# Performance work log

Hardware: AMD Instinct MI355X
Metric: run time of the kernel (lower is better)

The kernel has to match this reference:

```python
import jax, jax.numpy as jnp
import numpy as np

B, C, H, W = 8, 256, 64, 64
S = H * W  # dim_spatial = 4096
DQK = 256
DV = 256


def setup_inputs() -> dict:
    key = jax.random.key(0)
    k1, k2, k3, k4, k5 = jax.random.split(key, 5)
    queries = jax.random.normal(k1, (B, DQK, H, W), dtype=jnp.float32)
    keys = jax.random.normal(k2, (B, DQK, H, W), dtype=jnp.float32)
    values = jax.random.normal(k3, (B, DV, H, W), dtype=jnp.float32)
    q_pos = jax.random.normal(k4, (1, S, DQK), dtype=jnp.float32) * 0.05  # 'random_normal' init
    k_pos = jax.random.normal(k5, (1, S, DQK), dtype=jnp.float32) * 0.05
    return {"queries": queries, "keys": keys, "values": values, "q_pos": q_pos, "k_pos": k_pos}


def reference(queries, keys, values, q_pos, k_pos):
    scale = DQK ** (-0.5)
    # NCHW -> (B, S, C)
    q = jnp.transpose(queries, (0, 2, 3, 1)).reshape(-1, S, DQK) + q_pos
    k = jnp.transpose(keys, (0, 2, 3, 1)).reshape(-1, S, DQK) + k_pos
    v = jnp.transpose(values, (0, 2, 3, 1)).reshape(-1, S, DV)
    dots = jnp.einsum('bqd,bkd->bqk', q, k) * scale  # (B, S, S)
    attn = jax.nn.softmax(dots, axis=-1)
    out = jnp.einsum('bqk,bkd->bqd', attn, v)  # (B, S, DV)
    out = jnp.transpose(out, (0, 2, 1)).reshape(values.shape)  # (B, DV, H, W)
    return out
```

## Files before the change

### kernel.cpp

```cpp
#include <hip/hip_runtime.h>
#include <hip/hip_bf16.h>

#define B_N   8
#define S_N   4096
#define D_N   256
#define QBLK  128
#define KVBLK 32
#define NCH   (S_N / KVBLK)
#define IMGSZ 16384
#define SCALE_Q (0.0625f * 1.4426950408889634f)

typedef __attribute__((ext_vector_type(8)))  short bf16x8;
typedef __attribute__((ext_vector_type(16))) float f32x16;

__device__ __forceinline__ void async16(const char* g, char* l) {
  __builtin_amdgcn_global_load_lds(
      (const __attribute__((address_space(1))) void*)g,
      (__attribute__((address_space(3))) void*)l, 16, 0, 0);
}

__device__ __forceinline__ unsigned cvt_pk_bf16(float lo, float hi) {
  unsigned r;
  asm("v_cvt_pk_bf16_f32 %0, %1, %2" : "=v"(r) : "v"(lo), "v"(hi));
  return r;
}
__device__ __forceinline__ void swap32(unsigned& a, unsigned& b) {
  asm("v_permlane32_swap_b32 %0, %1" : "+v"(a), "+v"(b));
}
__device__ __forceinline__ float xhalf_max(float x) {
  float a = x, b = x;
  asm("" : "+v"(b));
  asm("v_permlane32_swap_b32 %0, %1" : "+v"(a), "+v"(b));
  return fmaxf(a, b);
}
__device__ __forceinline__ float xhalf_add(float x) {
  float a = x, b = x;
  asm("" : "+v"(b));
  asm("v_permlane32_swap_b32 %0, %1" : "+v"(a), "+v"(b));
  return a + b;
}
__device__ __forceinline__ float exp2_fast(float x) {
  float r;
  asm("v_exp_f32 %0, %1" : "=v"(r) : "v"(x));
  return r;
}
__device__ __forceinline__ unsigned short bf16_bits(float x) {
  union { __hip_bfloat16 h; unsigned short u; } cvt;
  cvt.h = __float2bfloat16(x);
  return cvt.u;
}

__global__ void prep_qk(const float* __restrict__ src, const float* __restrict__ pos,
                        __hip_bfloat16* __restrict__ dst, float mul) {
  __shared__ float tile[64][65];
  const int b  = blockIdx.z;
  const int s0 = blockIdx.x * 64;
  const int c0 = blockIdx.y * 64;
  const int t  = threadIdx.x;
  const int x  = t & 63;
  const int y4 = t >> 6;
  const float* sp = src + ((size_t)b * D_N + c0) * S_N + s0;
#pragma unroll
  for (int i = 0; i < 16; ++i) {
    int c = y4 + i * 4;
    tile[c][x] = sp[(size_t)c * S_N + x];
  }
  __syncthreads();
  __hip_bfloat16* dp = dst + ((size_t)b * S_N + s0) * D_N + c0;
  const float* pp = pos + (size_t)s0 * D_N + c0;
#pragma unroll
  for (int i = 0; i < 16; ++i) {
    int s = y4 + i * 4;
    float v = (tile[x][s] + pp[(size_t)s * D_N + x]) * mul;
    dp[(size_t)s * D_N + x] = __float2bfloat16(v);
  }
}

__global__ void prep_kimg(const float* __restrict__ src, const float* __restrict__ pos,
                          char* __restrict__ img) {
  __shared__ float tile[64][65];
  const int b  = blockIdx.z;
  const int s0 = blockIdx.x * 64;
  const int c0 = blockIdx.y * 64;
  const int t  = threadIdx.x;
  const int x  = t & 63;
  const int y4 = t >> 6;
  const float* sp = src + ((size_t)b * D_N + c0) * S_N + s0;
#pragma unroll
  for (int i = 0; i < 16; ++i) {
    int c = y4 + i * 4;
    tile[c][x] = sp[(size_t)c * S_N + x];
  }
  __syncthreads();
  const float* pp = pos + (size_t)s0 * D_N + c0;
#pragma unroll
  for (int i = 0; i < 16; ++i) {
    int srow = y4 + i * 4;
    int d    = c0 + x;
    float v  = tile[x][srow] + pp[(size_t)srow * D_N + x];
    int s    = s0 + srow;
    int ch   = s >> 5;
    char* dst = img + ((size_t)(b * NCH + ch)) * IMGSZ
                + (d >> 4) * 1024 + (s & 31) * 32 + (d & 15) * 2;
    *reinterpret_cast<__hip_bfloat16*>(dst) = __float2bfloat16(v);
  }
}

struct alignas(16) bf8s { __hip_bfloat16 v[8]; };
__global__ void prep_vimg(const float* __restrict__ src, char* __restrict__ img) {
  const int ch = blockIdx.x;
  const int b  = blockIdx.y;
  const int t  = threadIdx.x;
  char* ib = img + ((size_t)(b * NCH + ch)) * IMGSZ;
#pragma unroll
  for (int i = 0; i < 4; ++i) {
    int idx = i * 256 + t;
    int kf  = idx >> 9;
    int d   = (idx >> 1) & 255;
    int hf  = idx & 1;
    const float* vs = src + ((size_t)b * D_N + d) * S_N + ch * KVBLK + kf * 16 + hf * 8;
    float4 a = *reinterpret_cast<const float4*>(vs);
    float4 c = *reinterpret_cast<const float4*>(vs + 4);
    bf8s w;
    w.v[0] = __float2bfloat16(a.x); w.v[1] = __float2bfloat16(a.y);
    w.v[2] = __float2bfloat16(a.z); w.v[3] = __float2bfloat16(a.w);
    w.v[4] = __float2bfloat16(c.x); w.v[5] = __float2bfloat16(c.y);
    w.v[6] = __float2bfloat16(c.z); w.v[7] = __float2bfloat16(c.w);
    *reinterpret_cast<bf8s*>(ib + kf * 8192 + d * 32 + hf * 16) = w;
  }
}

#define LDS_BYTES 65536

__global__ __launch_bounds__(256, 2) void attn_kernel(
    const __hip_bfloat16* __restrict__ Qb, const char* __restrict__ Kt,
    const char* __restrict__ Vt, __hip_bfloat16* __restrict__ P0,
    float2* __restrict__ mlbuf, float* __restrict__ out) {
  __shared__ __align__(16) char lds[LDS_BYTES];

  const int tid  = threadIdx.x;
  const int wave = tid >> 6;
  const int lane = tid & 63;
  const int l31  = lane & 31;
  const int h    = lane >> 5;
  const int lofs = l31 * 32 + h * 16;

  const int lin = blockIdx.x;
  const int b   = lin & 7;
  const int kvh = (lin >> 3) & 1;
  const int qt  = lin >> 4;
  const int q0  = qt * QBLK + wave * 32;
  const int t0  = kvh * (NCH / 2);

  bf16x8 qf[16];
  {
    const __hip_bfloat16* qp = Qb + ((size_t)b * S_N + q0 + l31) * D_N + h * 8;
#pragma unroll
    for (int kc = 0; kc < 16; ++kc)
      qf[kc] = *reinterpret_cast<const bf16x8*>(qp + kc * 16);
  }

  f32x16 o[8];
#pragma unroll
  for (int df = 0; df < 8; ++df)
#pragma unroll
    for (int r = 0; r < 16; ++r) o[df][r] = 0.f;
  float m_ = -1e30f, l_ = 0.f;

  const char* kimgB = Kt + (size_t)b * NCH * IMGSZ;
  const char* vimgB = Vt + (size_t)b * NCH * IMGSZ;

  auto COMPUTE = [&](const char* Kbase, const char* Vbase) {
    f32x16 se;
#pragma unroll
    for (int r = 0; r < 16; ++r) se[r] = 0.f;
    {
      const char* kr = Kbase + lofs;
      __builtin_amdgcn_s_setprio(1);
#pragma unroll
      for (int kc = 0; kc < 16; ++kc) {
        bf16x8 kf8 = *reinterpret_cast<const bf16x8*>(kr + kc * 1024);
        se = __builtin_amdgcn_mfma_f32_32x32x16_bf16(kf8, qf[kc], se, 0, 0, 0);
      }
      __builtin_amdgcn_s_setprio(0);
    }

    float t8[8];
#pragma unroll
    for (int i = 0; i < 8; ++i) t8[i] = fmaxf(se[i], se[i + 8]);
    float pm = fmaxf(fmaxf(fmaxf(t8[0], t8[1]), fmaxf(t8[2], t8[3])),
                     fmaxf(fmaxf(t8[4], t8[5]), fmaxf(t8[6], t8[7])));
    float pmax = xhalf_max(pm);

    if (!__all(pmax <= m_ + 11.54f)) {
      float mn = fmaxf(m_, pmax);
      float al = exp2_fast(m_ - mn);
      m_ = mn;
      l_ *= al;
#pragma unroll
      for (int df = 0; df < 8; ++df)
#pragma unroll
        for (int r = 0; r < 16; ++r) o[df][r] *= al;
    }
#pragma unroll
    for (int r = 0; r < 16; ++r) se[r] = exp2_fast(se[r] - m_);
    float s8[8];
#pragma unroll
    for (int i = 0; i < 8; ++i) s8[i] = se[i] + se[i + 8];
    float rs = ((s8[0] + s8[1]) + (s8[2] + s8[3])) + ((s8[4] + s8[5]) + (s8[6] + s8[7]));
    l_ += xhalf_add(rs);

    union U8 { unsigned u[4]; bf16x8 v; };
    U8 pb[2];
    {
      unsigned u0 = cvt_pk_bf16(se[0],  se[1]);
      unsigned v0 = cvt_pk_bf16(se[4],  se[5]);
      swap32(u0, v0);
      unsigned u1 = cvt_pk_bf16(se[2],  se[3]);
      unsigned v1 = cvt_pk_bf16(se[6],  se[7]);
      swap32(u1, v1);
      pb[0].u[0] = u0; pb[0].u[1] = u1; pb[0].u[2] = v0; pb[0].u[3] = v1;
      unsigned u2 = cvt_pk_bf16(se[8],  se[9]);
      unsigned v2 = cvt_pk_bf16(se[12], se[13]);
      swap32(u2, v2);
      unsigned u3 = cvt_pk_bf16(se[10], se[11]);
      unsigned v3 = cvt_pk_bf16(se[14], se[15]);
      swap32(u3, v3);
      pb[1].u[0] = u2; pb[1].u[1] = u3; pb[1].u[2] = v2; pb[1].u[3] = v3;
    }

    {
      const char* vr = Vbase + lofs;
      __builtin_amdgcn_s_setprio(1);
#pragma unroll
      for (int df = 0; df < 8; ++df) {
        bf16x8 vf0 = *reinterpret_cast<const bf16x8*>(vr + df * 1024);
        bf16x8 vf1 = *reinterpret_cast<const bf16x8*>(vr + 8192 + df * 1024);
        o[df] = __builtin_amdgcn_mfma_f32_32x32x16_bf16(vf0, pb[0].v, o[df], 0, 0, 0);
        o[df] = __builtin_amdgcn_mfma_f32_32x32x16_bf16(vf1, pb[1].v, o[df], 0, 0, 0);
      }
      __builtin_amdgcn_s_setprio(0);
    }
  };

  for (int t = 0; t < NCH / 4; ++t) {
    __syncthreads();
    {
      const int ch = t0 + 2 * t + (wave & 1);
      const char* s = (wave < 2 ? kimgB : vimgB) + (size_t)ch * IMGSZ;
      char* dstb = lds + (wave < 2 ? 0 : 32768) + (wave & 1) * 16384;
#pragma unroll
      for (int c = 0; c < 16; ++c)
        async16(s + c * 1024 + lane * 16, dstb + c * 1024);
    }
    __syncthreads();

    COMPUTE(lds,         lds + 32768);
    COMPUTE(lds + 16384, lds + 49152);
  }

  if (h == 0)
    mlbuf[(size_t)(kvh * B_N + b) * S_N + q0 + l31] = make_float2(m_, l_);
  if (kvh) {
    float* pdst = out + (size_t)b * D_N * S_N + q0 + l31;
#pragma unroll
    for (int df = 0; df < 8; ++df)
#pragma unroll
      for (int r = 0; r < 16; ++r) {
        int d = df * 32 + (r & 3) + 8 * (r >> 2) + 4 * h;
        __builtin_nontemporal_store(o[df][r], pdst + (size_t)d * S_N);
      }
  } else {
    unsigned short* pdst = reinterpret_cast<unsigned short*>(P0)
                           + (size_t)b * D_N * S_N + q0 + l31;
#pragma unroll
    for (int df = 0; df < 8; ++df)
#pragma unroll
      for (int r = 0; r < 16; ++r) {
        int d = df * 32 + (r & 3) + 8 * (r >> 2) + 4 * h;
        __builtin_nontemporal_store(bf16_bits(o[df][r]), pdst + (size_t)d * S_N);
      }
  }
}

__global__ void merge_w(const float2* __restrict__ mlbuf, float2* __restrict__ wbuf) {
  int i = blockIdx.x * 256 + threadIdx.x;
  float2 a = mlbuf[i];
  float2 c = mlbuf[(size_t)B_N * S_N + i];
  float ms = fmaxf(a.x, c.x);
  float c0 = exp2f(a.x - ms), c1 = exp2f(c.x - ms);
  float inv = 1.0f / (c0 * a.y + c1 * c.y);
  wbuf[i] = make_float2(c0 * inv, c1 * inv);
}

__global__ void merge_o(const __hip_bfloat16* __restrict__ P0,
                        const float2* __restrict__ wbuf, float* __restrict__ out) {
  int i = blockIdx.x * 256 + threadIdx.x;
  ushort4 p0u = reinterpret_cast<const ushort4*>(P0)[i];
  float4 p1 = reinterpret_cast<float4*>(out)[i];
  int b  = i >> 18;
  int s4 = i & (S_N / 4 - 1);
  const float2* wb = wbuf + (size_t)b * S_N + s4 * 4;
  float2 w0 = wb[0], w1 = wb[1], w2 = wb[2], w3 = wb[3];
  union { unsigned short u; __hip_bfloat16 h; } cvt;
  float4 r;
  cvt.u = p0u.x; r.x = w0.x * __bfloat162float(cvt.h) + w0.y * p1.x;
  cvt.u = p0u.y; r.y = w1.x * __bfloat162float(cvt.h) + w1.y * p1.y;
  cvt.u = p0u.z; r.z = w2.x * __bfloat162float(cvt.h) + w2.y * p1.z;
  cvt.u = p0u.w; r.w = w3.x * __bfloat162float(cvt.h) + w3.y * p1.w;
  reinterpret_cast<float4*>(out)[i] = r;
}

extern "C" void kernel_launch(void* const* d_in, const int* in_sizes, int n_in,
                              void* d_out, int out_size, void* d_ws, size_t ws_size,
                              hipStream_t stream) {
  const float* queries = (const float*)d_in[0];
  const float* keys    = (const float*)d_in[1];
  const float* values  = (const float*)d_in[2];
  const float* q_pos   = (const float*)d_in[3];
  const float* k_pos   = (const float*)d_in[4];
  float* out = (float*)d_out;

  const size_t per = (size_t)B_N * S_N * D_N;
  __hip_bfloat16* Qb = (__hip_bfloat16*)d_ws;
  char*   Kt    = (char*)d_ws + per * 2;
  char*   Vt    = Kt + per * 2;
  __hip_bfloat16* P0 = (__hip_bfloat16*)(Vt + per * 2);
  float2* mlbuf = (float2*)((char*)P0 + per * 2);
  float2* wbuf  = mlbuf + (size_t)2 * B_N * S_N;

  prep_qk  <<<dim3(S_N / 64, D_N / 64, B_N), 256, 0, stream>>>(queries, q_pos, Qb, SCALE_Q);
  prep_kimg<<<dim3(S_N / 64, D_N / 64, B_N), 256, 0, stream>>>(keys,    k_pos, Kt);
  prep_vimg<<<dim3(NCH, B_N), 256, 0, stream>>>(values, Vt);
  attn_kernel<<<dim3((S_N / QBLK) * B_N * 2), 256, 0, stream>>>(Qb, Kt, Vt, P0, mlbuf, out);
  merge_w<<<dim3(B_N * S_N / 256), 256, 0, stream>>>(mlbuf, wbuf);
  merge_o<<<dim3((unsigned)(per / 4 / 256)), 256, 0, stream>>>(P0, wbuf, out);
}
```

Baseline: 192.5 us.

## Read V fragments directly from global memory and fuse merge weight computation

The attention kernel now stages only the K tiles in LDS and loads V operand fragments straight from global memory (through L2) inside the PV matmul, which halves LDS use from 64KB to 32KB. Freeing LDS could allow more blocks per CU, at the cost of exposing global-load latency directly in front of the PV MFMAs. The priority boost around the PV loop is also removed. The separate merge_w kernel is folded into merge_o, which now recomputes the rescale weights per element from the saved max/sum pairs, removing one launch and the intermediate weight buffer.

```diff
diff --git a/kernel.cpp b/kernel.cpp
--- a/kernel.cpp
+++ b/kernel.cpp
@@ -130,7 +130,7 @@
   }
 }
 
-#define LDS_BYTES 65536
+#define LDS_BYTES 32768
 
 __global__ __launch_bounds__(256, 2) void attn_kernel(
     const __hip_bfloat16* __restrict__ Qb, const char* __restrict__ Kt,
@@ -170,7 +170,7 @@
   const char* kimgB = Kt + (size_t)b * NCH * IMGSZ;
   const char* vimgB = Vt + (size_t)b * NCH * IMGSZ;
 
-  auto COMPUTE = [&](const char* Kbase, const char* Vbase) {
+  auto COMPUTE = [&](const char* Kbase, const char* vg) {
     f32x16 se;
 #pragma unroll
     for (int r = 0; r < 16; ++r) se[r] = 0.f;
@@ -230,8 +230,7 @@
     }
 
     {
-      const char* vr = Vbase + lofs;
-      __builtin_amdgcn_s_setprio(1);
+      const char* vr = vg + lofs;
 #pragma unroll
       for (int df = 0; df < 8; ++df) {
         bf16x8 vf0 = *reinterpret_cast<const bf16x8*>(vr + df * 1024);
@@ -239,24 +238,23 @@
         o[df] = __builtin_amdgcn_mfma_f32_32x32x16_bf16(vf0, pb[0].v, o[df], 0, 0, 0);
         o[df] = __builtin_amdgcn_mfma_f32_32x32x16_bf16(vf1, pb[1].v, o[df], 0, 0, 0);
       }
-      __builtin_amdgcn_s_setprio(0);
     }
   };
 
   for (int t = 0; t < NCH / 4; ++t) {
     __syncthreads();
     {
-      const int ch = t0 + 2 * t + (wave & 1);
-      const char* s = (wave < 2 ? kimgB : vimgB) + (size_t)ch * IMGSZ;
-      char* dstb = lds + (wave < 2 ? 0 : 32768) + (wave & 1) * 16384;
-#pragma unroll
-      for (int c = 0; c < 16; ++c)
-        async16(s + c * 1024 + lane * 16, dstb + c * 1024);
+      const char* s = kimgB + (size_t)(t0 + 2 * t) * IMGSZ;
+#pragma unroll
+      for (int c = 0; c < 8; ++c) {
+        int seg = wave * 8 + c;
+        async16(s + seg * 1024 + lane * 16, lds + seg * 1024);
+      }
     }
     __syncthreads();
 
-    COMPUTE(lds,         lds + 32768);
-    COMPUTE(lds + 16384, lds + 49152);
+    COMPUTE(lds,         vimgB + (size_t)(t0 + 2 * t)     * IMGSZ);
+    COMPUTE(lds + 16384, vimgB + (size_t)(t0 + 2 * t + 1) * IMGSZ);
   }
 
   if (h == 0)
@@ -283,32 +281,31 @@
   }
 }
 
-__global__ void merge_w(const float2* __restrict__ mlbuf, float2* __restrict__ wbuf) {
-  int i = blockIdx.x * 256 + threadIdx.x;
-  float2 a = mlbuf[i];
-  float2 c = mlbuf[(size_t)B_N * S_N + i];
-  float ms = fmaxf(a.x, c.x);
-  float c0 = exp2f(a.x - ms), c1 = exp2f(c.x - ms);
-  float inv = 1.0f / (c0 * a.y + c1 * c.y);
-  wbuf[i] = make_float2(c0 * inv, c1 * inv);
-}
-
 __global__ void merge_o(const __hip_bfloat16* __restrict__ P0,
-                        const float2* __restrict__ wbuf, float* __restrict__ out) {
+                        const float2* __restrict__ mlbuf, float* __restrict__ out) {
   int i = blockIdx.x * 256 + threadIdx.x;
   ushort4 p0u = reinterpret_cast<const ushort4*>(P0)[i];
   float4 p1 = reinterpret_cast<float4*>(out)[i];
   int b  = i >> 18;
   int s4 = i & (S_N / 4 - 1);
-  const float2* wb = wbuf + (size_t)b * S_N + s4 * 4;
-  float2 w0 = wb[0], w1 = wb[1], w2 = wb[2], w3 = wb[3];
+  const float2* ml0 = mlbuf + (size_t)b * S_N + s4 * 4;
+  const float2* ml1 = ml0 + (size_t)B_N * S_N;
   union { unsigned short u; __hip_bfloat16 h; } cvt;
-  float4 r;
-  cvt.u = p0u.x; r.x = w0.x * __bfloat162float(cvt.h) + w0.y * p1.x;
-  cvt.u = p0u.y; r.y = w1.x * __bfloat162float(cvt.h) + w1.y * p1.y;
-  cvt.u = p0u.z; r.z = w2.x * __bfloat162float(cvt.h) + w2.y * p1.z;
-  cvt.u = p0u.w; r.w = w3.x * __bfloat162float(cvt.h) + w3.y * p1.w;
-  reinterpret_cast<float4*>(out)[i] = r;
+  float r[4], p0f[4];
+  cvt.u = p0u.x; p0f[0] = __bfloat162float(cvt.h);
+  cvt.u = p0u.y; p0f[1] = __bfloat162float(cvt.h);
+  cvt.u = p0u.z; p0f[2] = __bfloat162float(cvt.h);
+  cvt.u = p0u.w; p0f[3] = __bfloat162float(cvt.h);
+  float p1f[4] = {p1.x, p1.y, p1.z, p1.w};
+#pragma unroll
+  for (int j = 0; j < 4; ++j) {
+    float2 a = ml0[j], c = ml1[j];
+    float ms = fmaxf(a.x, c.x);
+    float c0 = exp2f(a.x - ms), c1 = exp2f(c.x - ms);
+    float inv = 1.0f / (c0 * a.y + c1 * c.y);
+    r[j] = (c0 * p0f[j] + c1 * p1f[j]) * inv;
+  }
+  reinterpret_cast<float4*>(out)[i] = make_float4(r[0], r[1], r[2], r[3]);
 }
 
 extern "C" void kernel_launch(void* const* d_in, const int* in_sizes, int n_in,
@@ -327,12 +324,10 @@
   char*   Vt    = Kt + per * 2;
   __hip_bfloat16* P0 = (__hip_bfloat16*)(Vt + per * 2);
   float2* mlbuf = (float2*)((char*)P0 + per * 2);
-  float2* wbuf  = mlbuf + (size_t)2 * B_N * S_N;
 
   prep_qk  <<<dim3(S_N / 64, D_N / 64, B_N), 256, 0, stream>>>(queries, q_pos, Qb, SCALE_Q);
   prep_kimg<<<dim3(S_N / 64, D_N / 64, B_N), 256, 0, stream>>>(keys,    k_pos, Kt);
   prep_vimg<<<dim3(NCH, B_N), 256, 0, stream>>>(values, Vt);
   attn_kernel<<<dim3((S_N / QBLK) * B_N * 2), 256, 0, stream>>>(Qb, Kt, Vt, P0, mlbuf, out);
-  merge_w<<<dim3(B_N * S_N / 256), 256, 0, stream>>>(mlbuf, wbuf);
-  merge_o<<<dim3((unsigned)(per / 4 / 256)), 256, 0, stream>>>(P0, wbuf, out);
-}
+  merge_o<<<dim3((unsigned)(per / 4 / 256)), 256, 0, stream>>>(P0, mlbuf, out);
+}
```

Measured after the change: 273.0 us. 41.8% more time.
